# Kernel tuning notes

Measured on AMD Instinct MI355X. Metric: run time of the kernel, lower is better.

## Reference

```python
import jax, jax.numpy as jnp
import numpy as np


def setup_inputs() -> dict:
    key = jax.random.key(0)
    k1, k2 = jax.random.split(key)
    B, F, Ci, R = 16, 1024, 64, 1
    Co, K = 64, 4
    ll = jax.random.normal(k1, (B, F, Ci, R), dtype=jnp.float32)
    logits = jax.random.normal(k2, (Co, Ci, K, K, R), dtype=jnp.float32)
    return {"ll": ll, "logits": logits}


def reference(ll, logits):
    # ll: (B, F, Ci, R)   logits: (Co, Ci, K, K, R)
    B, F, Ci, R = ll.shape
    Co, _, K, _, _ = logits.shape
    H = W = int(F ** 0.5)
    OH, OW = H // K, W // K
    # normalize weights over input channels (sum_dim=1)
    lw = jax.nn.log_softmax(logits, axis=1)  # (Co, Ci, K, K, R)
    # b (h w) ci r -> b ci h w r
    x = ll.reshape(B, H, W, Ci, R).transpose(0, 3, 1, 2, 4)
    # b ci (oh kh) (ow kw) r -> b ci oh ow kh kw r
    x = x.reshape(B, Ci, OH, K, OW, K, R).transpose(0, 1, 2, 4, 3, 5, 6)
    # broadcast-add log-weights (shared over oh, ow) then logsumexp over ci
    weighted = x[:, None] + lw[None, :, :, None, None, :, :, :]  # (B, Co, Ci, OH, OW, K, K, R)
    res = jax.scipy.special.logsumexp(weighted, axis=2)          # (B, Co, OH, OW, K, K, R)
    # b co oh ow kh kw r -> b (oh kh ow kw) co r
    out = res.transpose(0, 2, 4, 3, 5, 1, 6).reshape(B, F, Co, R)
    return out
```

## Files before the change

kernel.cpp:

```cpp
#include <hip/hip_runtime.h>

#define CI 64
#define CO 64
#define B_ 16
#define F_ 1024
#define W_IMG 32
#define KK 4
#define NPAT 16
#define BLOCKS_PER_PAT 32
#define PAIRS_PER_PAT 1024
#define PAIRS_PER_BLOCK (PAIRS_PER_PAT / BLOCKS_PER_PAT)
#define PAIRS_PER_WAVE (PAIRS_PER_BLOCK / 4)

__global__ __launch_bounds__(256, 2) void sumconv_kernel(
    const float* __restrict__ ll,
    const float* __restrict__ logits,
    float* __restrict__ out)
{
    __shared__ float Wl[CI * CO];
    __shared__ float part[4 * CO];
    __shared__ float lsum_s[CO];
    __shared__ float p_lds[4][CI];

    const int tid   = threadIdx.x;
    const int lane  = tid & 63;
    const int wv    = tid >> 6;
    const int bid   = blockIdx.x;
    const int pat   = bid & (NPAT - 1);
    const int chunk = bid >> 4;

    {
        const int co = lane;
        const float* lg = logits + co * (CI * KK * KK) + pat;
        float psum = 0.f;
        #pragma unroll
        for (int i = 0; i < 16; ++i) {
            const int ci = wv * 16 + i;
            const float e = __expf(lg[ci * (KK * KK)]);
            Wl[ci * CO + co] = e;
            psum += e;
        }
        part[wv * CO + co] = psum;
    }
    __syncthreads();
    if (wv == 0) {
        const float tot = (part[lane] + part[CO + lane])
                        + (part[2 * CO + lane] + part[3 * CO + lane]);
        lsum_s[lane] = __logf(tot);
    }
    __syncthreads();

    float wreg[CI];
    #pragma unroll
    for (int ci = 0; ci < CI; ++ci) wreg[ci] = Wl[ci * CO + lane];
    const float lsum = lsum_s[lane];

    const int kh = pat >> 2;
    const int kw = pat & 3;

    #pragma unroll 1
    for (int j = 0; j < PAIRS_PER_WAVE; ++j) {
        const int pr = chunk * PAIRS_PER_BLOCK + wv * PAIRS_PER_WAVE + j;
        const int b  = pr >> 6;
        const int oh = (pr >> 3) & 7;
        const int ow = pr & 7;
        const int f  = (oh * 4 + kh) * W_IMG + (ow * 4 + kw);
        const int idx = (b * F_ + f) * CI + lane;

        const float x = ll[idx];
        const float p = __expf(x);
        p_lds[wv][lane] = p;

        float a0 = 0.f, a1 = 0.f, a2 = 0.f, a3 = 0.f;
        #pragma unroll
        for (int ci = 0; ci < CI; ci += 4) {
            const float4 pv = *reinterpret_cast<const float4*>(&p_lds[wv][ci]);
            a0 = fmaf(pv.x, wreg[ci + 0], a0);
            a1 = fmaf(pv.y, wreg[ci + 1], a1);
            a2 = fmaf(pv.z, wreg[ci + 2], a2);
            a3 = fmaf(pv.w, wreg[ci + 3], a3);
        }
        out[idx] = __logf((a0 + a1) + (a2 + a3)) - lsum;
    }
}

extern "C" void kernel_launch(void* const* d_in, const int* in_sizes, int n_in,
                              void* d_out, int out_size, void* d_ws, size_t ws_size,
                              hipStream_t stream) {
    const float* ll     = (const float*)d_in[0];
    const float* logits = (const float*)d_in[1];
    float* out          = (float*)d_out;
    sumconv_kernel<<<dim3(NPAT * BLOCKS_PER_PAT), dim3(256), 0, stream>>>(ll, logits, out);
}
```

Baseline: 70.89 us.

## Split weight exp-normalization into prep kernel and batch four pixels per wave

The exp/log-sum-exp preprocessing of the logits moves out of every block into a small prep kernel that writes exp-weights and log-sums to workspace. The main kernel then launches 1024 blocks, each wave handling four pixels. Their ll loads are issued up front and the four dot products are interleaved, which raises memory-level parallelism and ILP. The cost is a second launch plus global reads of the 16KB weight slice per block in place of recomputing it locally.

```diff
diff --git a/kernel.cpp b/kernel.cpp
--- a/kernel.cpp
+++ b/kernel.cpp
@@ -2,86 +2,89 @@
 
 #define CI 64
 #define CO 64
-#define B_ 16
 #define F_ 1024
-#define W_IMG 32
 #define KK 4
 #define NPAT 16
-#define BLOCKS_PER_PAT 32
-#define PAIRS_PER_PAT 1024
-#define PAIRS_PER_BLOCK (PAIRS_PER_PAT / BLOCKS_PER_PAT)
-#define PAIRS_PER_WAVE (PAIRS_PER_BLOCK / 4)
 
-__global__ __launch_bounds__(256, 2) void sumconv_kernel(
-    const float* __restrict__ ll,
-    const float* __restrict__ logits,
-    float* __restrict__ out)
+__global__ __launch_bounds__(256) void prep_kernel(
+    const float* __restrict__ logits, float* __restrict__ E, float* __restrict__ Lsum)
 {
-    __shared__ float Wl[CI * CO];
     __shared__ float part[4 * CO];
-    __shared__ float lsum_s[CO];
-    __shared__ float p_lds[4][CI];
+    const int pat = blockIdx.x;
+    const int t   = threadIdx.x;
+    const int co  = t & 63;
+    const int q   = t >> 6;
+    const float* lg = logits + co * (CI * KK * KK) + pat;
+    float psum = 0.f;
+    #pragma unroll
+    for (int i = 0; i < 16; ++i) {
+        const int ci = q * 16 + i;
+        const float e = __expf(lg[ci * (KK * KK)]);
+        E[pat * (CI * CO) + ci * CO + co] = e;
+        psum += e;
+    }
+    part[q * CO + co] = psum;
+    __syncthreads();
+    if (q == 0) {
+        const float tot = (part[co] + part[CO + co]) + (part[2 * CO + co] + part[3 * CO + co]);
+        Lsum[pat * CO + co] = __logf(tot);
+    }
+}
 
+__global__ __launch_bounds__(256, 4) void main_kernel(
+    const float* __restrict__ ll, const float* __restrict__ E,
+    const float* __restrict__ Lsum, float* __restrict__ out)
+{
+    __shared__ float p_lds[4][4][CI];
     const int tid   = threadIdx.x;
     const int lane  = tid & 63;
     const int wv    = tid >> 6;
     const int bid   = blockIdx.x;
     const int pat   = bid & (NPAT - 1);
     const int chunk = bid >> 4;
+    const int kh = pat >> 2, kw = pat & 3;
 
-    {
-        const int co = lane;
-        const float* lg = logits + co * (CI * KK * KK) + pat;
-        float psum = 0.f;
-        #pragma unroll
-        for (int i = 0; i < 16; ++i) {
-            const int ci = wv * 16 + i;
-            const float e = __expf(lg[ci * (KK * KK)]);
-            Wl[ci * CO + co] = e;
-            psum += e;
-        }
-        part[wv * CO + co] = psum;
-    }
-    __syncthreads();
-    if (wv == 0) {
-        const float tot = (part[lane] + part[CO + lane])
-                        + (part[2 * CO + lane] + part[3 * CO + lane]);
-        lsum_s[lane] = __logf(tot);
-    }
-    __syncthreads();
-
-    float wreg[CI];
+    int   idx[4];
+    float p[4];
     #pragma unroll
-    for (int ci = 0; ci < CI; ++ci) wreg[ci] = Wl[ci * CO + lane];
-    const float lsum = lsum_s[lane];
-
-    const int kh = pat >> 2;
-    const int kw = pat & 3;
-
-    #pragma unroll 1
-    for (int j = 0; j < PAIRS_PER_WAVE; ++j) {
-        const int pr = chunk * PAIRS_PER_BLOCK + wv * PAIRS_PER_WAVE + j;
+    for (int j = 0; j < 4; ++j) {
+        const int pr = (chunk << 4) + (wv << 2) + j;
         const int b  = pr >> 6;
         const int oh = (pr >> 3) & 7;
         const int ow = pr & 7;
-        const int f  = (oh * 4 + kh) * W_IMG + (ow * 4 + kw);
-        const int idx = (b * F_ + f) * CI + lane;
+        const int f  = (oh * 4 + kh) * 32 + (ow * 4 + kw);
+        idx[j] = (b * F_ + f) * CI + lane;
+        p[j]   = ll[idx[j]];
+    }
 
-        const float x = ll[idx];
-        const float p = __expf(x);
-        p_lds[wv][lane] = p;
+    const float* Ep = E + pat * (CI * CO) + lane;
+    float wreg[CI];
+    #pragma unroll
+    for (int ci = 0; ci < CI; ++ci) wreg[ci] = Ep[ci * CO];
+    const float lsum = Lsum[pat * CO + lane];
 
-        float a0 = 0.f, a1 = 0.f, a2 = 0.f, a3 = 0.f;
+    #pragma unroll
+    for (int j = 0; j < 4; ++j) {
+        p[j] = __expf(p[j]);
+        p_lds[wv][j][lane] = p[j];
+    }
+    __builtin_amdgcn_wave_barrier();
+
+    float a0[4] = {0.f, 0.f, 0.f, 0.f}, a1[4] = {0.f, 0.f, 0.f, 0.f};
+    #pragma unroll
+    for (int ci = 0; ci < CI; ci += 4) {
         #pragma unroll
-        for (int ci = 0; ci < CI; ci += 4) {
-            const float4 pv = *reinterpret_cast<const float4*>(&p_lds[wv][ci]);
-            a0 = fmaf(pv.x, wreg[ci + 0], a0);
-            a1 = fmaf(pv.y, wreg[ci + 1], a1);
-            a2 = fmaf(pv.z, wreg[ci + 2], a2);
-            a3 = fmaf(pv.w, wreg[ci + 3], a3);
+        for (int j = 0; j < 4; ++j) {
+            const float4 pv = *reinterpret_cast<const float4*>(&p_lds[wv][j][ci]);
+            a0[j] = fmaf(pv.x, wreg[ci + 0], a0[j]);
+            a1[j] = fmaf(pv.y, wreg[ci + 1], a1[j]);
+            a0[j] = fmaf(pv.z, wreg[ci + 2], a0[j]);
+            a1[j] = fmaf(pv.w, wreg[ci + 3], a1[j]);
         }
-        out[idx] = __logf((a0 + a1) + (a2 + a3)) - lsum;
     }
+    #pragma unroll
+    for (int j = 0; j < 4; ++j)
+        out[idx[j]] = __logf(a0[j] + a1[j]) - lsum;
 }
 
 extern "C" void kernel_launch(void* const* d_in, const int* in_sizes, int n_in,
@@ -89,6 +92,9 @@
                               hipStream_t stream) {
     const float* ll     = (const float*)d_in[0];
     const float* logits = (const float*)d_in[1];
-    float* out          = (float*)d_out;
-    sumconv_kernel<<<dim3(NPAT * BLOCKS_PER_PAT), dim3(256), 0, stream>>>(ll, logits, out);
+    float* out  = (float*)d_out;
+    float* E    = (float*)d_ws;
+    float* Lsum = E + NPAT * CI * CO;
+    prep_kernel<<<dim3(NPAT), dim3(256), 0, stream>>>(logits, E, Lsum);
+    main_kernel<<<dim3(1024), dim3(256), 0, stream>>>(ll, E, Lsum, out);
 }
```

After: 64.97 us. 1.09x faster.
